# Optimization experiments

Measured on AMD Instinct MI355X. Metric: run time of the kernel, lower is better.

## Reference

```python
import jax, jax.numpy as jnp
import numpy as np

B, S, T = 64, 128, 32
VOCAB, N_ENT, N_REL = 50000, 200000, 500
IN_DIM, KG_DIM, H, C = 300, 100, 256, 3


def setup_inputs() -> dict:
    key = jax.random.key(0)
    ks = jax.random.split(key, 16)
    inputs = jax.random.randint(ks[0], (B, S), 0, VOCAB)
    head = jax.random.randint(ks[1], (B, S, T, 1), 0, N_ENT)
    tail = jax.random.randint(ks[2], (B, S, T, 1), 0, N_ENT)
    rel = jax.random.randint(ks[3], (B, S, T, 1), 0, N_REL)
    triples = jnp.concatenate([head, tail, rel], axis=-1)  # [B,S,T,3]
    lengths = jax.random.randint(ks[4], (B,), 1, S + 1)
    # values in {-1,0,1}; a token row of all -1 means "no KG triples" (torch.equal branch)
    id2_ids_batch = jax.random.randint(ks[5], (B, S, T), 0, 3) - 1
    s = 0.02
    word_emb = jax.random.normal(ks[6], (VOCAB, IN_DIM)) * s
    ent_emb = jax.random.normal(ks[7], (N_ENT, KG_DIM)) * s
    rel_emb = jax.random.normal(ks[8], (N_REL, KG_DIM)) * s
    W_ent = jax.random.normal(ks[9], (KG_DIM, 2 * KG_DIM)) * s  # entity_transformed (no bias)
    w_ih = jax.random.normal(ks[10], (4 * H, IN_DIM + 2 * KG_DIM)) * s
    w_hh = jax.random.normal(ks[11], (4 * H, H)) * s
    b_ih = jnp.zeros((4 * H,), jnp.float32)
    b_hh = jnp.zeros((4 * H,), jnp.float32)
    W_att = jax.random.normal(ks[12], (1, H)) * s
    b_att = jax.random.normal(ks[13], (1,)) * s
    W_out = jax.random.normal(ks[14], (C, H)) * s
    b_out = jnp.zeros((C,), jnp.float32)
    return dict(inputs=inputs, triples=triples, lengths=lengths, id2_ids_batch=id2_ids_batch,
                word_emb=word_emb, ent_emb=ent_emb, rel_emb=rel_emb, W_ent=W_ent,
                w_ih=w_ih, w_hh=w_hh, b_ih=b_ih, b_hh=b_hh,
                W_att=W_att, b_att=b_att, W_out=W_out, b_out=b_out)


def reference(inputs, triples, lengths, id2_ids_batch, word_emb, ent_emb, rel_emb,
              W_ent, w_ih, w_hh, b_ih, b_hh, W_att, b_att, W_out, b_out):
    x = word_emb[inputs]                                   # [B,S,IN]
    head = ent_emb[triples[..., 0]]                        # [B,S,T,D]
    tail = ent_emb[triples[..., 1]]
    rel = rel_emb[triples[..., 2]]
    head_tail = jnp.concatenate([head, tail], axis=-1)     # [B,S,T,2D]
    # entity_transformed + tanh; relation side only gets tanh (relation_transformed
    # linear is defined but never applied in the original forward — preserved).
    ht_tr = jnp.tanh(jnp.einsum('bstk,dk->bstd', head_tail, W_ent))
    e = jnp.sum(ht_tr * jnp.tanh(rel), axis=-1)            # [B,S,T]
    alpha = jax.nn.softmax(e, axis=-1)                     # softmax over triples
    graph_embed = jnp.einsum('bst,bstk->bsk', alpha, head_tail)  # [B,S,2D]
    valid = jnp.any(id2_ids_batch != -1, axis=-1)          # torch.equal(-1) branches
    graph_embed = jnp.where(valid[..., None], graph_embed, 0.0)
    t = jnp.concatenate([x, graph_embed], axis=-1)         # [B,S,IN+2D]

    def step(carry, xt):
        h, c = carry
        gates = xt @ w_ih.T + h @ w_hh.T + b_ih + b_hh
        i, f, g, o = jnp.split(gates, 4, axis=-1)          # PyTorch gate order
        c = jax.nn.sigmoid(f) * c + jax.nn.sigmoid(i) * jnp.tanh(g)
        h = jax.nn.sigmoid(o) * jnp.tanh(c)
        return (h, c), h

    h0 = jnp.zeros((t.shape[0], w_hh.shape[1]), t.dtype)
    _, hs = jax.lax.scan(step, (h0, h0), jnp.swapaxes(t, 0, 1))  # [S,B,H]
    output = jnp.swapaxes(hs, 0, 1)                               # [B,S,H]
    # pad_packed_sequence -> zeros past each sequence length
    len_mask = jnp.arange(S)[None, :] < lengths[:, None]
    output = output * len_mask[..., None].astype(output.dtype)

    logits = (output @ W_att.T + b_att)[..., 0]            # [B,S]
    mask = (logits != 0).astype(output.dtype)
    # AllenNLP-style last_dim_softmax with mask
    p = jax.nn.softmax(logits * mask, axis=-1) * mask
    p = p / (jnp.sum(p, axis=-1, keepdims=True) + 1e-13)
    enc = jnp.einsum('bs,bsh->bh', p, output)              # [B,H]
    log_probs = jax.nn.log_softmax(enc @ W_out.T + b_out, axis=-1)
    return log_probs, p
```

## Files before the change

kernel.cpp:

```cpp
#include <hip/hip_runtime.h>


typedef unsigned short ushort_t;
typedef unsigned char uchar_t;
typedef __bf16 bf16x8 __attribute__((ext_vector_type(8)));
typedef float f32x4 __attribute__((ext_vector_type(4)));
typedef int i32x4 __attribute__((ext_vector_type(4)));

#define NENT 200000
#define NVOC 50000
#define NREL 500
#define KPAD 512

__device__ __forceinline__ float b2f(ushort_t u) {
    return __uint_as_float(((unsigned)u) << 16);
}
__device__ __forceinline__ ushort_t f2b(float f) {
    unsigned u = __float_as_uint(f);
    unsigned r = (u + 0x7FFFu + ((u >> 16) & 1u)) >> 16;
    return (ushort_t)r;
}
__device__ __forceinline__ float sigm(float x) {
    return __builtin_amdgcn_rcpf(1.f + __expf(-x));
}
__device__ __forceinline__ float tanh_fast(float x) {
    float xx = fminf(fmaxf(x, -15.f), 15.f);
    float t = __expf(2.f * xx);
    return 1.f - 2.f * __builtin_amdgcn_rcpf(t + 1.f);
}
__device__ __forceinline__ int iacc(const void* p, long long i, int di) {
    return di ? ((const int*)p)[2 * i] : ((const int*)p)[i];
}

__global__ void k_sentinel(float* __restrict__ out, int n, float val) {
    int i = blockIdx.x * 256 + threadIdx.x;
    if (i < n) out[i] = val;
}

__global__ void k_det(const int* __restrict__ triples, unsigned* __restrict__ dflag) {
    __shared__ int cnt;
    int tid = threadIdx.x;
    if (tid == 0) cnt = 0;
    __syncthreads();
    int nz = 0;
    for (int i = tid; i < 1500; i += 256)
        if (triples[2 * i + 1] != 0) nz++;
    if (nz) atomicAdd(&cnt, nz);
    __syncthreads();
    if (tid == 0) *dflag = (cnt == 0) ? 2u : 0u;
}

__global__ void k_prep(const float* __restrict__ Went, const float* __restrict__ wih,
                       const float* __restrict__ relE,
                       ushort_t* __restrict__ Wb, ushort_t* __restrict__ wihT,
                       float* __restrict__ trelP) {
    int i = blockIdx.x * 256 + threadIdx.x;
    int stride = gridDim.x * 256;
    if (i < 112 * 256) {
        int n = i >> 8, k = i & 255;
        float v = 0.f;
        if (n < 100) {
            if (k < 100) v = Went[n * 200 + k];
            else if (k >= 128 && k < 228) v = Went[n * 200 + 100 + (k - 128)];
        }
        Wb[i] = f2b(v);
    }
    for (int j = i; j < 500 * 128; j += stride) {
        int r_ = j >> 7, d = j & 127;
        if (d < 112) trelP[r_ * 112 + d] = (d < 100) ? tanhf(relE[r_ * 100 + d]) : 0.f;
    }
    for (int j = i; j < 512 * 1024; j += stride) {
        int k = j >> 10, n = j & 1023;
        wihT[j] = (k < 500) ? f2b(wih[(long long)n * 500 + k]) : (ushort_t)0;
    }
}

__global__ void k_prep2(const float* __restrict__ whh, uchar_t* __restrict__ whhI8) {
    int j = blockIdx.x * 256 + threadIdx.x;
    int f = j >> 10, r = j & 1023;
    int lane = r >> 4, jj = r & 15;
    int ntg = f >> 2, kt = f & 3;
    int np = ntg * 16 + (lane & 15);
    int k = kt * 64 + ((lane >> 4) << 4) + jj;
    int u = np >> 2, gg = np & 3;
    int qv = __float2int_rn(whh[(gg * 256 + u) * 256 + k] * 1024.f);
    qv = min(max(qv, -127), 127);
    whhI8[j] = (uchar_t)(qv & 0xFF);
}

__global__ __launch_bounds__(128) void k_graph(const void* __restrict__ inputs,
                                               const void* __restrict__ triples,
                                               const void* __restrict__ id2,
                                               const float* __restrict__ wordE,
                                               const float* __restrict__ entE,
                                               const ushort_t* __restrict__ Wb,
                                               const float* __restrict__ trelP,
                                               ushort_t* __restrict__ tfeat,
                                               const unsigned* __restrict__ dflag) {
    int di = ((*dflag) >> 1) & 1;
    int bs = blockIdx.x;
    int tid = threadIdx.x;
    __shared__ __align__(16) ushort_t As[32][256];
    __shared__ int rids[32];
    __shared__ float e_sm[32];
    __shared__ float alpha[32];
    __shared__ int vflag;
    if (tid == 0) vflag = 0;
    __syncthreads();
    int t = tid >> 2, l4 = tid & 3;
    long long base3 = ((long long)bs * 32 + t) * 3;
    int hid = iacc(triples, base3, di);
    int tl = iacc(triples, base3 + 1, di);
    int rid = iacc(triples, base3 + 2, di);
    hid = min(max(hid, 0), NENT - 1);
    tl = min(max(tl, 0), NENT - 1);
    rid = min(max(rid, 0), NREL - 1);
    if (l4 == 0) {
        rids[t] = rid;
        if (iacc(id2, (long long)bs * 32 + t, di) != -1) vflag = 1;
    }
    for (int k = l4; k < 256; k += 4) {
        float v = 0.f;
        if (k < 100) v = entE[(long long)hid * 100 + k];
        else if (k >= 128 && k < 228) v = entE[(long long)tl * 100 + (k - 128)];
        As[t][k] = f2b(v);
    }
    __syncthreads();
    int wave = tid >> 6, lane = tid & 63, m16 = lane & 15, q = lane >> 4;
    f32x4 acc[7];
#pragma unroll
    for (int nt = 0; nt < 7; nt++) acc[nt] = {0.f, 0.f, 0.f, 0.f};
#pragma unroll
    for (int ks = 0; ks < 8; ++ks) {
        bf16x8 af = *reinterpret_cast<const bf16x8*>(&As[wave * 16 + m16][ks * 32 + q * 8]);
#pragma unroll
        for (int nt = 0; nt < 7; ++nt) {
            bf16x8 bf_ = *reinterpret_cast<const bf16x8*>(&Wb[(nt * 16 + m16) * 256 + ks * 32 + q * 8]);
            acc[nt] = __builtin_amdgcn_mfma_f32_16x16x32_bf16(af, bf_, acc[nt], 0, 0, 0);
        }
    }
#pragma unroll
    for (int rr = 0; rr < 4; ++rr) {
        int m = wave * 16 + q * 4 + rr;
        const float* tr = trelP + rids[m] * 112;
        float s = 0.f;
#pragma unroll
        for (int nt = 0; nt < 7; ++nt) s += tanhf(acc[nt][rr]) * tr[nt * 16 + m16];
        s += __shfl_xor(s, 1);
        s += __shfl_xor(s, 2);
        s += __shfl_xor(s, 4);
        s += __shfl_xor(s, 8);
        if (m16 == 0) e_sm[m] = s;
    }
    __syncthreads();
    if (tid < 32) {
        float v = e_sm[tid];
        float mx = v;
        for (int off = 16; off >= 1; off >>= 1) mx = fmaxf(mx, __shfl_xor(mx, off));
        float ex = __expf(v - mx);
        float sm = ex;
        for (int off = 16; off >= 1; off >>= 1) sm += __shfl_xor(sm, off);
        alpha[tid] = ex / sm;
    }
    __syncthreads();
    float scale = vflag ? 1.f : 0.f;
    long long row = (long long)bs * KPAD;
    for (int k = tid; k < 200; k += 128) {
        int kk = (k < 100) ? k : (k + 28);
        float ge = 0.f;
#pragma unroll 8
        for (int tt = 0; tt < 32; ++tt) ge += alpha[tt] * b2f(As[tt][kk]);
        tfeat[row + 300 + k] = f2b(ge * scale);
    }
    int w = iacc(inputs, bs, di);
    w = min(max(w, 0), NVOC - 1);
    for (int j = tid; j < 300; j += 128) tfeat[row + j] = f2b(wordE[(long long)w * 300 + j]);
    if (tid < 12) tfeat[row + 500 + tid] = 0;
}

__global__ __launch_bounds__(256) void k_gemm_xw(const ushort_t* __restrict__ A,
                                                 const ushort_t* __restrict__ Bm,
                                                 const float* __restrict__ bih,
                                                 const float* __restrict__ bhh,
                                                 ushort_t* __restrict__ xwB) {
    __shared__ __align__(16) ushort_t As[64 * 32];
    __shared__ __align__(16) ushort_t Bs[64 * 32];
    int tid = threadIdx.x;
    int i0 = blockIdx.x * 64, n0 = blockIdx.y * 64;
    int wave = tid >> 6, lane = tid & 63, m16 = lane & 15, q = lane >> 4;
    f32x4 acc[4];
#pragma unroll
    for (int t = 0; t < 4; t++) acc[t] = {0.f, 0.f, 0.f, 0.f};
    int r = tid >> 2, cq = (tid & 3) * 8;
    int kk = tid >> 3, nn = (tid & 7) * 8;
    for (int kt = 0; kt < 16; ++kt) {
        int k0 = kt * 32;
        {
            const ushort_t* src = A + (i0 + r) * 512 + k0 + cq;
            ushort4 v0 = *(const ushort4*)src;
            ushort4 v1 = *(const ushort4*)(src + 4);
            *(ushort4*)&As[r * 32 + cq] = v0;
            *(ushort4*)&As[r * 32 + cq + 4] = v1;
        }
        {
            const ushort_t* src = Bm + (k0 + kk) * 1024 + n0 + nn;
            ushort4 v0 = *(const ushort4*)(src);
            ushort4 v1 = *(const ushort4*)(src + 4);
            Bs[(nn + 0) * 32 + kk] = v0.x; Bs[(nn + 1) * 32 + kk] = v0.y;
            Bs[(nn + 2) * 32 + kk] = v0.z; Bs[(nn + 3) * 32 + kk] = v0.w;
            Bs[(nn + 4) * 32 + kk] = v1.x; Bs[(nn + 5) * 32 + kk] = v1.y;
            Bs[(nn + 6) * 32 + kk] = v1.z; Bs[(nn + 7) * 32 + kk] = v1.w;
        }
        __syncthreads();
        bf16x8 af = *reinterpret_cast<const bf16x8*>(&As[(wave * 16 + m16) * 32 + q * 8]);
#pragma unroll
        for (int t = 0; t < 4; t++) {
            bf16x8 bf_ = *reinterpret_cast<const bf16x8*>(&Bs[(t * 16 + m16) * 32 + q * 8]);
            acc[t] = __builtin_amdgcn_mfma_f32_16x16x32_bf16(af, bf_, acc[t], 0, 0, 0);
        }
        __syncthreads();
    }
#pragma unroll
    for (int t = 0; t < 4; t++) {
        int n = n0 + t * 16 + m16;
        float bias = bih[n] + bhh[n];
        int ni = ((n & 255) << 2) + (n >> 8);
#pragma unroll
        for (int rr = 0; rr < 4; rr++) {
            int i = i0 + wave * 16 + q * 4 + rr;
            xwB[i * 1024 + ni] = f2b(acc[t][rr] + bias);
        }
    }
}

__global__ __launch_bounds__(512, 2) void k_lstm(const ushort_t* __restrict__ xwB,
                                                 const uchar_t* __restrict__ whhI8,
                                                 const void* __restrict__ lengths,
                                                 ushort_t* __restrict__ hallB,
                                                 const unsigned* __restrict__ dflag) {
    const int LDH = 272;
    int di = ((*dflag) >> 1) & 1;
    int b = blockIdx.x;
    int tid = threadIdx.x;
    int wave = tid >> 6, lane = tid & 63;
    int c16 = lane & 15, q = lane >> 4;
    __shared__ __align__(16) uchar_t hsm[16 * 272];
    __shared__ __align__(16) float gbuf[1024];
    for (int j = tid; j < 16 * 272; j += 512) hsm[j] = 0;
    i32x4 wreg[8][4];
    {
        const uchar_t* wp = whhI8 + (((long long)(wave * 8) * 4) * 64 + lane) * 16;
#pragma unroll
        for (int i = 0; i < 8; ++i)
#pragma unroll
            for (int kt = 0; kt < 4; ++kt)
                wreg[i][kt] = *(const i32x4*)(wp + (((i << 2) + kt) << 10));
    }
    int len = iacc(lengths, b, di);
    int u = tid;
    float cc = 0.f;
    const float S = 1.f / (127.f * 1024.f);
    long long xbase = ((long long)(b * 128) << 10) + ((long long)u << 2);
    ushort4 xv = {0, 0, 0, 0}, xn;
    if (tid < 256) xv = *(const ushort4*)(xwB + xbase);
    __syncthreads();
    for (int s = 0; s < 128; ++s) {
        const uchar_t* hb = &hsm[c16 * LDH];
        i32x4 afr[4];
#pragma unroll
        for (int kt = 0; kt < 4; ++kt)
            afr[kt] = *(const i32x4*)(hb + kt * 64 + q * 16);
        int sn = (s < 127) ? s + 1 : 127;
        if (tid < 256) xn = *(const ushort4*)(xwB + xbase + ((long long)sn << 10));
#pragma unroll
        for (int i = 0; i < 8; ++i) {
            i32x4 a = {0, 0, 0, 0};
#pragma unroll
            for (int kt = 0; kt < 4; ++kt)
                a = __builtin_amdgcn_mfma_i32_16x16x64_i8(afr[kt], wreg[i][kt], a, 0, 0, 0);
            if (q == 0) gbuf[(wave * 8 + i) * 16 + c16] = (float)a[0];
        }
        asm volatile("s_waitcnt lgkmcnt(0)\n\ts_barrier" ::: "memory");
        if (tid < 256) {
            f32x4 gv = *(const f32x4*)&gbuf[u * 4];
            float iv = b2f(xv.x) + gv[0] * S;
            float fv = b2f(xv.y) + gv[1] * S;
            float gg = b2f(xv.z) + gv[2] * S;
            float ov = b2f(xv.w) + gv[3] * S;
            float c = sigm(fv) * cc + sigm(iv) * tanh_fast(gg);
            float h = sigm(ov) * tanh_fast(c);
            cc = c;
            hsm[u] = (uchar_t)(__float2int_rn(h * 127.f) & 0xFF);
            hallB[((long long)(b * 128 + s) << 8) + u] = (s < len) ? f2b(h) : (ushort_t)0;
            xv = xn;
        }
        asm volatile("s_waitcnt lgkmcnt(0)\n\ts_barrier" ::: "memory");
    }
}

__global__ __launch_bounds__(256) void k_att(const ushort_t* __restrict__ hallB,
                                             const float* __restrict__ Watt,
                                             const float* __restrict__ batt,
                                             const float* __restrict__ Wout,
                                             const float* __restrict__ bout,
                                             float* __restrict__ out) {
    int b = blockIdx.x, tid = threadIdx.x;
    __shared__ float waf[256], lg[128], msk[128], ps[128], enc[256], o3[3], red[1];
    waf[tid] = Watt[tid];
    __syncthreads();
    int s = tid >> 1, half = tid & 1;
    const ushort_t* hb = hallB + (b * 128 + s) * 256 + half * 128;
    float part = 0.f;
    for (int j = 0; j < 128; ++j) part += b2f(hb[j]) * waf[half * 128 + j];
    part += __shfl_xor(part, 1);
    if (half == 0) lg[s] = part + batt[0];
    __syncthreads();
    if (tid < 128) {
        float lv = lg[tid];
        float m = (lv != 0.f) ? 1.f : 0.f;
        msk[tid] = m;
        lg[tid] = lv * m;
    }
    __syncthreads();
    if (tid == 0) {
        float mx = -1e30f;
        for (int i = 0; i < 128; ++i) mx = fmaxf(mx, lg[i]);
        red[0] = mx;
    }
    __syncthreads();
    if (tid < 128) ps[tid] = __expf(lg[tid] - red[0]);
    __syncthreads();
    if (tid == 0) {
        float sm = 0.f;
        for (int i = 0; i < 128; ++i) sm += ps[i];
        red[0] = sm;
    }
    __syncthreads();
    if (tid < 128) ps[tid] = ps[tid] / red[0] * msk[tid];
    __syncthreads();
    if (tid == 0) {
        float sm = 0.f;
        for (int i = 0; i < 128; ++i) sm += ps[i];
        red[0] = sm + 1e-13f;
    }
    __syncthreads();
    if (tid < 128) {
        float p = ps[tid] / red[0];
        ps[tid] = p;
        out[192 + b * 128 + tid] = p;
    }
    __syncthreads();
    {
        float ej = 0.f;
        for (int ss = 0; ss < 128; ++ss) ej += ps[ss] * b2f(hallB[(b * 128 + ss) * 256 + tid]);
        enc[tid] = ej;
    }
    __syncthreads();
    if (tid < 3) {
        float a = 0.f;
        for (int j = 0; j < 256; ++j) a += enc[j] * Wout[tid * 256 + j];
        o3[tid] = a + bout[tid];
    }
    __syncthreads();
    if (tid == 0) {
        float m = fmaxf(o3[0], fmaxf(o3[1], o3[2]));
        float l = logf(__expf(o3[0] - m) + __expf(o3[1] - m) + __expf(o3[2] - m)) + m;
        out[b * 3 + 0] = o3[0] - l;
        out[b * 3 + 1] = o3[1] - l;
        out[b * 3 + 2] = o3[2] - l;
    }
}

extern "C" void kernel_launch(void* const* d_in, const int* in_sizes, int n_in,
                              void* d_out, int out_size, void* d_ws, size_t ws_size,
                              hipStream_t stream) {
    float* out = (float*)d_out;
    static const long long EXP[16] = {8192, 786432, 64, 262144, 15000000, 20000000,
                                      50000, 20000, 512000, 262144, 1024, 1024,
                                      256, 1, 768, 3};
    int ob = (out_size + 255) / 256;
    if (n_in != 16 || out_size != 8384) {
        hipLaunchKernelGGL(k_sentinel, dim3(ob), dim3(256), 0, stream, out, out_size, -8192.f);
        return;
    }
    for (int i = 0; i < 16; ++i) {
        if ((long long)in_sizes[i] != EXP[i]) {
            hipLaunchKernelGGL(k_sentinel, dim3(ob), dim3(256), 0, stream, out, out_size,
                               -(4096.f + 32.f * i));
            return;
        }
    }

    const void* inputs = d_in[0];
    const void* triples = d_in[1];
    const void* lengths = d_in[2];
    const void* id2 = d_in[3];
    const float* wordE = (const float*)d_in[4];
    const float* entE = (const float*)d_in[5];
    const float* relE = (const float*)d_in[6];
    const float* Went = (const float*)d_in[7];
    const float* wih = (const float*)d_in[8];
    const float* whh = (const float*)d_in[9];
    const float* bih = (const float*)d_in[10];
    const float* bhh = (const float*)d_in[11];
    const float* Watt = (const float*)d_in[12];
    const float* batt = (const float*)d_in[13];
    const float* Wout = (const float*)d_in[14];
    const float* bout = (const float*)d_in[15];
    char* ws = (char*)d_ws;

    constexpr size_t OFF_XW = 0;
    constexpr size_t OFF_TFEAT = 16777216;
    constexpr size_t OFF_WIHT = 25165824;
    constexpr size_t OFF_WB = 26214400;
    constexpr size_t OFF_FLAGS = 26271744;
    constexpr size_t OFF_TRELP = 26272000;
    constexpr size_t WS_NEEDED = 26496000;

    if (ws_size < WS_NEEDED) {
        hipLaunchKernelGGL(k_sentinel, dim3(ob), dim3(256), 0, stream, out, out_size,
                           -(float)(ws_size >> 20));
        return;
    }

    ushort_t* xwB = (ushort_t*)(ws + OFF_XW);
    ushort_t* tfeat = (ushort_t*)(ws + OFF_TFEAT);
    ushort_t* hallB = (ushort_t*)(ws + OFF_TFEAT);
    ushort_t* wihT = (ushort_t*)(ws + OFF_WIHT);
    uchar_t* whhI8 = (uchar_t*)(ws + OFF_WIHT);
    ushort_t* Wb = (ushort_t*)(ws + OFF_WB);
    unsigned* dflag = (unsigned*)(ws + OFF_FLAGS);
    float* trelP = (float*)(ws + OFF_TRELP);

    hipLaunchKernelGGL(k_det, dim3(1), dim3(256), 0, stream, (const int*)triples, dflag);
    hipLaunchKernelGGL(k_prep, dim3(2048), dim3(256), 0, stream,
                       Went, wih, relE, Wb, wihT, trelP);
    hipLaunchKernelGGL(k_graph, dim3(8192), dim3(128), 0, stream,
                       inputs, triples, id2, wordE, entE, Wb, trelP, tfeat, dflag);
    hipLaunchKernelGGL(k_gemm_xw, dim3(128, 16), dim3(256), 0, stream,
                       tfeat, wihT, bih, bhh, xwB);
    hipLaunchKernelGGL(k_prep2, dim3(1024), dim3(256), 0, stream, whh, whhI8);
    hipLaunchKernelGGL(k_lstm, dim3(64), dim3(512), 0, stream, xwB, whhI8, lengths, hallB, dflag);
    hipLaunchKernelGGL(k_att, dim3(64), dim3(256), 0, stream, hallB, Watt, batt, Wout, bout, out);
}
```

Baseline: 551.3 us.

## Restructure k_graph entity gather with coalesced float2 loads and swizzled LDS

Reworks the entity embedding gather in k_graph. Wave 0 now reads the triple indices once, and the other wave zeroes the padding. Each 100-float entity row is then loaded by one wave as coalesced float2 reads packed into bf16 pairs and stored into an XOR-swizzled LDS tile, which should reduce bank conflicts on the MFMA fragment loads. It also swaps tanhf for a fast exp-based tanh and vectorizes the word-embedding copy. The gather loop is meant to replace scattered per-thread scalar loads and to cut LDS conflicts, at some cost in tanh precision.

```diff
diff --git a/kernel.cpp b/kernel.cpp
--- a/kernel.cpp
+++ b/kernel.cpp
@@ -11,6 +11,7 @@
 #define NVOC 50000
 #define NREL 500
 #define KPAD 512
+#define ASW(t, k) ((((t) * 512 + (k) * 2)) ^ (((t) & 7) << 4))
 
 __device__ __forceinline__ float b2f(ushort_t u) {
     return __uint_as_float(((unsigned)u) << 16);
@@ -100,39 +101,50 @@
     int di = ((*dflag) >> 1) & 1;
     int bs = blockIdx.x;
     int tid = threadIdx.x;
-    __shared__ __align__(16) ushort_t As[32][256];
-    __shared__ int rids[32];
-    __shared__ float e_sm[32];
-    __shared__ float alpha[32];
+    __shared__ __align__(16) uchar_t As[32 * 512];
+    __shared__ int hid_sm[32], tl_sm[32], rids[32];
+    __shared__ float e_sm[32], alpha[32];
     __shared__ int vflag;
-    if (tid == 0) vflag = 0;
-    __syncthreads();
-    int t = tid >> 2, l4 = tid & 3;
-    long long base3 = ((long long)bs * 32 + t) * 3;
-    int hid = iacc(triples, base3, di);
-    int tl = iacc(triples, base3 + 1, di);
-    int rid = iacc(triples, base3 + 2, di);
-    hid = min(max(hid, 0), NENT - 1);
-    tl = min(max(tl, 0), NENT - 1);
-    rid = min(max(rid, 0), NREL - 1);
-    if (l4 == 0) {
-        rids[t] = rid;
-        if (iacc(id2, (long long)bs * 32 + t, di) != -1) vflag = 1;
-    }
-    for (int k = l4; k < 256; k += 4) {
-        float v = 0.f;
-        if (k < 100) v = entE[(long long)hid * 100 + k];
-        else if (k >= 128 && k < 228) v = entE[(long long)tl * 100 + (k - 128)];
-        As[t][k] = f2b(v);
-    }
-    __syncthreads();
-    int wave = tid >> 6, lane = tid & 63, m16 = lane & 15, q = lane >> 4;
+    int wave = tid >> 6, lane = tid & 63;
+
+    if (wave == 0) {
+        int idv = -1;
+        if (lane < 32) {
+            long long base3 = ((long long)bs * 32 + lane) * 3;
+            hid_sm[lane] = min(max(iacc(triples, base3, di), 0), NENT - 1);
+            tl_sm[lane] = min(max(iacc(triples, base3 + 1, di), 0), NENT - 1);
+            rids[lane] = min(max(iacc(triples, base3 + 2, di), 0), NREL - 1);
+            idv = iacc(id2, (long long)bs * 32 + lane, di);
+        }
+        unsigned long long bal = __ballot(idv != -1);
+        if (lane == 0) vflag = (bal != 0ULL) ? 1 : 0;
+    } else {
+        for (int j = lane; j < 32 * 14; j += 64) {
+            int t = j / 14, g = j % 14;
+            int c = (g < 7) ? (100 + g * 4) : (228 + (g - 7) * 4);
+            *(unsigned long long*)&As[ASW(t, c)] = 0ULL;
+        }
+    }
+    __syncthreads();
+#pragma unroll 4
+    for (int slot = wave; slot < 64; slot += 2) {
+        int t = slot & 31;
+        const float* src = entE + (long long)((slot < 32) ? hid_sm[t] : tl_sm[t]) * 100;
+        int cb = (slot < 32) ? 0 : 128;
+        if (lane < 50) {
+            float2 v = *(const float2*)(src + 2 * lane);
+            unsigned pk = ((unsigned)f2b(v.y) << 16) | (unsigned)f2b(v.x);
+            *(unsigned*)&As[ASW(t, cb + 2 * lane)] = pk;
+        }
+    }
+    __syncthreads();
+    int m16 = lane & 15, q = lane >> 4;
     f32x4 acc[7];
 #pragma unroll
     for (int nt = 0; nt < 7; nt++) acc[nt] = {0.f, 0.f, 0.f, 0.f};
 #pragma unroll
     for (int ks = 0; ks < 8; ++ks) {
-        bf16x8 af = *reinterpret_cast<const bf16x8*>(&As[wave * 16 + m16][ks * 32 + q * 8]);
+        bf16x8 af = *reinterpret_cast<const bf16x8*>(&As[ASW(wave * 16 + m16, ks * 32 + q * 8)]);
 #pragma unroll
         for (int nt = 0; nt < 7; ++nt) {
             bf16x8 bf_ = *reinterpret_cast<const bf16x8*>(&Wb[(nt * 16 + m16) * 256 + ks * 32 + q * 8]);
@@ -145,7 +157,7 @@
         const float* tr = trelP + rids[m] * 112;
         float s = 0.f;
 #pragma unroll
-        for (int nt = 0; nt < 7; ++nt) s += tanhf(acc[nt][rr]) * tr[nt * 16 + m16];
+        for (int nt = 0; nt < 7; ++nt) s += tanh_fast(acc[nt][rr]) * tr[nt * 16 + m16];
         s += __shfl_xor(s, 1);
         s += __shfl_xor(s, 2);
         s += __shfl_xor(s, 4);
@@ -169,12 +181,16 @@
         int kk = (k < 100) ? k : (k + 28);
         float ge = 0.f;
 #pragma unroll 8
-        for (int tt = 0; tt < 32; ++tt) ge += alpha[tt] * b2f(As[tt][kk]);
+        for (int tt = 0; tt < 32; ++tt)
+            ge += alpha[tt] * b2f(*(const ushort_t*)&As[ASW(tt, kk)]);
         tfeat[row + 300 + k] = f2b(ge * scale);
     }
-    int w = iacc(inputs, bs, di);
-    w = min(max(w, 0), NVOC - 1);
-    for (int j = tid; j < 300; j += 128) tfeat[row + j] = f2b(wordE[(long long)w * 300 + j]);
+    int w = min(max(iacc(inputs, bs, di), 0), NVOC - 1);
+    const float* wsrc = wordE + (long long)w * 300;
+    for (int j = tid; j < 150; j += 128) {
+        float2 v = *(const float2*)(wsrc + 2 * j);
+        *(unsigned*)&tfeat[row + 2 * j] = ((unsigned)f2b(v.y) << 16) | (unsigned)f2b(v.x);
+    }
     if (tid < 12) tfeat[row + 500 + tid] = 0;
 }
 
```

Result: faster. 508.8 us (-7.7%).
